# Kernel tuning notes

Measured on AMD Instinct MI355X. Metric: run time of the kernel, lower is better.

Reference implementation:

```python
import jax, jax.numpy as jnp
import numpy as np

B, DIM, HEADS, H, W = 4, 64, 64, 256, 256


def _conv1x1(x, w):
    # x: [b,c,h,w], w: [o,c] -> [b,o,h,w]
    return jnp.einsum('bchw,oc->bohw', x, w)


def _conv3x3_s2_reflect(x, w, groups):
    # reflect pad 1, 3x3 conv, stride 2 (matches padding_mode='reflect', stride=2)
    xp = jnp.pad(x, ((0, 0), (0, 0), (1, 1), (1, 1)), mode='reflect')
    return jax.lax.conv_general_dilated(
        xp, w, window_strides=(2, 2), padding='VALID',
        dimension_numbers=('NCHW', 'OIHW', 'NCHW'), feature_group_count=groups)


def _to_heads(t, heads):
    # safe_rearrange: zero-pad channels to a multiple of heads, then b (head c) h w -> b head c (h w)
    b, c, h, w = t.shape
    if c % heads != 0:
        t = jnp.pad(t, ((0, 0), (0, heads - c % heads), (0, 0), (0, 0)))
        c = t.shape[1]
    return t.reshape(b, heads, c // heads, h * w)


def _l2norm(t, eps=1e-12):
    # F.normalize(dim=-1): x / max(||x||, eps)
    n = jnp.sqrt(jnp.sum(t * t, axis=-1, keepdims=True))
    return t / jnp.maximum(n, eps)


def setup_inputs() -> dict:
    key = jax.random.key(0)
    ks = jax.random.split(key, 13)
    d = DIM
    s = 0.05
    return {
        'x': jax.random.normal(ks[0], (B, d, H, W), jnp.float32),
        'illu_feat': jax.random.uniform(ks[1], (B, d, H, W), jnp.float32),
        'w_q_spec': jax.random.normal(ks[2], (d, d), jnp.float32) * s,
        'w_k_spec': jax.random.normal(ks[3], (d, d), jnp.float32) * s,
        'w_v_spec': jax.random.normal(ks[4], (d, d), jnp.float32) * s,
        'w_q_spat': jax.random.normal(ks[5], (d, 1, 3, 3), jnp.float32) * s,  # depthwise
        'w_k_spat': jax.random.normal(ks[6], (d, d, 3, 3), jnp.float32) * s,
        'w_v_spat': jax.random.normal(ks[7], (d, d), jnp.float32) * s,
        'w_anchor_dw': jax.random.normal(ks[8], (d, 1, 3, 3), jnp.float32) * s,  # depthwise
        'w_anchor_pw': jax.random.normal(ks[9], (d // 2, d), jnp.float32) * s,
        'w_proj': jax.random.normal(ks[10], (d, d), jnp.float32) * s,
        'temp_spec': jnp.ones((HEADS, 1, 1), jnp.float32),
        'temp_spat': jnp.ones((HEADS, 1, 1), jnp.float32),
    }


def reference(x, illu_feat, w_q_spec, w_k_spec, w_v_spec, w_q_spat, w_k_spat,
              w_v_spat, w_anchor_dw, w_anchor_pw, w_proj, temp_spec, temp_spat):
    b, c, h, w = x.shape
    heads = HEADS

    q_spec = _conv1x1(x, w_q_spec)
    k_spec = _conv1x1(x, w_k_spec)                       # computed but unused downstream (as in original)
    v_spec = _conv1x1(x, w_v_spec) * illu_feat
    q_spat = _conv3x3_s2_reflect(x, w_q_spat, groups=c)  # computed but unused downstream (as in original)
    k_spat = _conv3x3_s2_reflect(x, w_k_spat, groups=1)
    v_spat = _conv1x1(x, w_v_spat) * illu_feat
    anchor = _conv1x1(_conv3x3_s2_reflect(x, w_anchor_dw, groups=c), w_anchor_pw)

    q_spec = _l2norm(_to_heads(q_spec, heads))
    k_spec = _l2norm(_to_heads(k_spec, heads))
    v_spec = _to_heads(v_spec, heads)
    q_spat = _l2norm(_to_heads(q_spat, heads))
    k_spat = _to_heads(k_spat, heads)
    v_spat = _to_heads(v_spat, heads)
    anchor = _l2norm(_to_heads(anchor, heads))

    n_q = q_spec.shape[-1]      # h*w
    n_a = anchor.shape[-1]      # (h//2)*(w//2)
    n_v = v_spec.shape[-1]
    n_k = k_spat.shape[-1]

    # spectral branch: q x anchor (truncate to common spatial length)
    m = min(n_q, n_a)
    attn_spec = jnp.einsum('bhcn,bhdn->bhcd', q_spec[..., :m], anchor[..., :m]) * temp_spec
    attn_spec = jax.nn.softmax(attn_spec, axis=-1)

    # v_spec spatial matching via adaptive avg pool (static no-op here since n_v == n_q)
    if n_v != n_q:
        vh = int(n_v ** 0.5)
        qh = int(n_q ** 0.5)
        v4 = v_spec.reshape(b, heads, v_spec.shape[2], vh, vh)
        v4 = jax.image.resize(v4, (b, heads, v_spec.shape[2], qh, qh), method='linear')
        v_spec_matched = v4.reshape(b, heads, v_spec.shape[2], -1)
    else:
        v_spec_matched = v_spec

    # spatial branch: anchor x k_spat (truncate to common spatial length)
    m2 = min(n_a, n_k)
    attn_spat = jnp.einsum('bhcn,bhdn->bhcd', anchor[..., :m2], k_spat[..., :m2]) * temp_spat
    attn_spat = jax.nn.softmax(attn_spat, axis=-1)

    out_spec = jnp.einsum('bhcd,bhdn->bhcn', attn_spec, v_spec_matched)
    out_spat = jnp.einsum('bhcd,bhdn->bhcn', attn_spat, v_spat)

    m3 = min(out_spec.shape[-1], out_spat.shape[-1])
    out = 0.6 * out_spec[..., :m3] + 0.4 * out_spat[..., :m3]

    ah = int(m3 ** 0.5)
    out = out.reshape(b, heads * out.shape[2], ah, ah)
    if ah != h or ah != w:
        # F.interpolate bilinear, align_corners=False == half-pixel linear resize
        out = jax.image.resize(out, (b, out.shape[1], h, w), method='bilinear')
    out = out[:, :DIM]
    return _conv1x1(out, w_proj)
```

## Files before the change

kernel.cpp:

```cpp
#include <hip/hip_runtime.h>


#define HW    65536
#define CHHW  (64 * 65536)
#define PT    128
#define SXT   68
#define SIL   132
#define TPB   4

typedef short s4_t __attribute__((ext_vector_type(4)));
typedef short s8_t __attribute__((ext_vector_type(8)));
typedef float f4_t __attribute__((ext_vector_type(4)));

static __device__ __forceinline__ unsigned short f2bf(float f) {
  unsigned u = __float_as_uint(f);
  return (unsigned short)((u + 0x7fffu + ((u >> 16) & 1u)) >> 16);
}
static __device__ __forceinline__ s8_t ld8(const unsigned short* p) {
  s4_t lo = *(const s4_t*)p;
  s4_t hi = *(const s4_t*)(p + 4);
  s8_t r = {lo[0], lo[1], lo[2], lo[3], hi[0], hi[1], hi[2], hi[3]};
  return r;
}

__global__ __launch_bounds__(256, 2) void fused_hsattn(
    const float* __restrict__ x, const float* __restrict__ illu,
    const float* __restrict__ wvs, const float* __restrict__ wvt,
    const float* __restrict__ wproj, float* __restrict__ out) {
  __shared__ __align__(16) unsigned short WM[64 * SXT];
  __shared__ __align__(16) unsigned short WP[64 * SXT];
  __shared__ __align__(16) unsigned short XT[PT * SXT];
  __shared__ __align__(16) float ILS[64 * SIL];

  const int tid  = threadIdx.x;
  const int lane = tid & 63;
  const int wv   = tid >> 6;
  const int n15  = lane & 15;
  const int q    = lane >> 4;

  const int ch0 = wv * 16 + (lane >> 5);
  const int pxl = (lane & 31) * 4;

  f4_t wa[4], wb[4], wc[4];
#pragma unroll
  for (int it = 0; it < 4; ++it) {
    int j4 = (it * 256 + tid) * 4;
    wa[it] = *(const f4_t*)(wvs + j4);
    wb[it] = *(const f4_t*)(wvt + j4);
    wc[it] = *(const f4_t*)(wproj + j4);
  }

  f4_t xr[8], ir[8];
  {
    const int g    = blockIdx.x * TPB;
    const int base = (g >> 9) * CHHW + ((g & 511) << 7);
#pragma unroll
    for (int it = 0; it < 8; ++it) {
      const int off = base + (ch0 + 2 * it) * HW + pxl;
      xr[it] = *(const f4_t*)(x + off);
      ir[it] = *(const f4_t*)(illu + off);
    }
  }

#pragma unroll
  for (int it = 0; it < 4; ++it) {
    int idx = it * 256 + tid;
    int r = idx >> 4, c4 = (idx & 15) * 4;
    s4_t m, w;
#pragma unroll
    for (int j = 0; j < 4; ++j) {
      m[j] = (short)f2bf(0.6f * wa[it][j] + 0.4f * wb[it][j]);
      w[j] = (short)f2bf(wc[it][j]);
    }
    *(s4_t*)(WM + r * SXT + c4) = m;
    *(s4_t*)(WP + r * SXT + c4) = w;
  }

#pragma unroll
  for (int t = 0; t < TPB; ++t) {
    const int g    = blockIdx.x * TPB + t;
    const int base = (g >> 9) * CHHW + ((g & 511) << 7);

#pragma unroll
    for (int it = 0; it < 8; ++it) {
      const int ch = ch0 + 2 * it;
      f4_t v = xr[it];
#pragma unroll
      for (int j = 0; j < 4; ++j)
        XT[(pxl + j) * SXT + ch] = f2bf(v[j]);
      *(f4_t*)(ILS + ch * SIL + pxl) = ir[it];
    }
    __syncthreads();

    if (t + 1 < TPB) {
      const int g2 = g + 1;
      const int b2 = (g2 >> 9) * CHHW + ((g2 & 511) << 7);
#pragma unroll
      for (int it = 0; it < 8; ++it) {
        const int off = b2 + (ch0 + 2 * it) * HW + pxl;
        xr[it] = *(const f4_t*)(x + off);
        ir[it] = *(const f4_t*)(illu + off);
      }
    }

#pragma unroll
    for (int nt = 0; nt < 2; ++nt) {
      const int pr = wv * 32 + nt * 16;
      unsigned short* xrow = XT + (pr + n15) * SXT;

      f4_t acc[4];
#pragma unroll
      for (int i = 0; i < 4; ++i) acc[i] = (f4_t){0.f, 0.f, 0.f, 0.f};
#pragma unroll
      for (int kc = 0; kc < 2; ++kc) {
        s8_t B = ld8(xrow + kc * 32 + q * 8);
#pragma unroll
        for (int mt = 0; mt < 4; ++mt) {
          s8_t A = ld8(WM + (mt * 16 + n15) * SXT + kc * 32 + q * 8);
          acc[mt] = __builtin_amdgcn_mfma_f32_16x16x32_bf16(A, B, acc[mt], 0, 0, 0);
        }
      }

#pragma unroll
      for (int mt = 0; mt < 4; ++mt) {
        s4_t h;
#pragma unroll
        for (int r = 0; r < 4; ++r) {
          const int c = mt * 16 + q * 4 + r;
          h[r] = (short)f2bf(acc[mt][r] * ILS[c * SIL + pr + n15]);
        }
        *(s4_t*)(xrow + mt * 16 + q * 4) = h;
      }

      f4_t acc2[4];
#pragma unroll
      for (int i = 0; i < 4; ++i) acc2[i] = (f4_t){0.f, 0.f, 0.f, 0.f};
#pragma unroll
      for (int kc = 0; kc < 2; ++kc) {
        s8_t B = ld8(xrow + kc * 32 + q * 8);
#pragma unroll
        for (int mt = 0; mt < 4; ++mt) {
          s8_t A = ld8(WP + (mt * 16 + n15) * SXT + kc * 32 + q * 8);
          acc2[mt] = __builtin_amdgcn_mfma_f32_16x16x32_bf16(A, B, acc2[mt], 0, 0, 0);
        }
      }

#pragma unroll
      for (int mt = 0; mt < 4; ++mt) {
        float* op = out + base + (mt * 16 + q * 4) * HW + pr + n15;
        f4_t a = acc2[mt];
#pragma unroll
        for (int r = 0; r < 4; ++r) op[r * HW] = a[r];
      }
    }
    __syncthreads();
  }
}

extern "C" void kernel_launch(void* const* d_in, const int* in_sizes, int n_in,
                              void* d_out, int out_size, void* d_ws, size_t ws_size,
                              hipStream_t stream) {
  const float* x     = (const float*)d_in[0];
  const float* illu  = (const float*)d_in[1];
  const float* wvs   = (const float*)d_in[4];
  const float* wvt   = (const float*)d_in[7];
  const float* wproj = (const float*)d_in[10];
  float* out = (float*)d_out;

  fused_hsattn<<<(4 * (HW / PT)) / TPB, 256, 0, stream>>>(x, illu, wvs, wvt,
                                                          wproj, out);
}
```

Measured before the change: 203.3 us.

## Load MFMA operands directly from global into registers, dropping shared staging

After: 252.7 us. +24.3%, slower.

```diff
diff --git a/kernel.cpp b/kernel.cpp
--- a/kernel.cpp
+++ b/kernel.cpp
@@ -3,10 +3,10 @@
 
 #define HW    65536
 #define CHHW  (64 * 65536)
-#define PT    128
 #define SXT   68
-#define SIL   132
-#define TPB   4
+#define WPX   32
+#define BPX   128
+#define TPB   2
 
 typedef short s4_t __attribute__((ext_vector_type(4)));
 typedef short s8_t __attribute__((ext_vector_type(8)));
@@ -23,23 +23,20 @@
   return r;
 }
 
-__global__ __launch_bounds__(256, 2) void fused_hsattn(
+__global__ __launch_bounds__(256, 4) void fused_hsattn(
     const float* __restrict__ x, const float* __restrict__ illu,
     const float* __restrict__ wvs, const float* __restrict__ wvt,
     const float* __restrict__ wproj, float* __restrict__ out) {
   __shared__ __align__(16) unsigned short WM[64 * SXT];
   __shared__ __align__(16) unsigned short WP[64 * SXT];
-  __shared__ __align__(16) unsigned short XT[PT * SXT];
-  __shared__ __align__(16) float ILS[64 * SIL];
+  __shared__ __align__(16) unsigned short XH[BPX * SXT];
 
   const int tid  = threadIdx.x;
   const int lane = tid & 63;
   const int wv   = tid >> 6;
   const int n15  = lane & 15;
   const int q    = lane >> 4;
-
-  const int ch0 = wv * 16 + (lane >> 5);
-  const int pxl = (lane & 31) * 4;
+  const int wpx  = wv * WPX;
 
   f4_t wa[4], wb[4], wc[4];
 #pragma unroll
@@ -48,18 +45,6 @@
     wa[it] = *(const f4_t*)(wvs + j4);
     wb[it] = *(const f4_t*)(wvt + j4);
     wc[it] = *(const f4_t*)(wproj + j4);
-  }
-
-  f4_t xr[8], ir[8];
-  {
-    const int g    = blockIdx.x * TPB;
-    const int base = (g >> 9) * CHHW + ((g & 511) << 7);
-#pragma unroll
-    for (int it = 0; it < 8; ++it) {
-      const int off = base + (ch0 + 2 * it) * HW + pxl;
-      xr[it] = *(const f4_t*)(x + off);
-      ir[it] = *(const f4_t*)(illu + off);
-    }
   }
 
 #pragma unroll
@@ -75,85 +60,112 @@
     *(s4_t*)(WM + r * SXT + c4) = m;
     *(s4_t*)(WP + r * SXT + c4) = w;
   }
+  __syncthreads();
+
+  unsigned short* xr0 = XH + (wpx + n15) * SXT;
+  unsigned short* xr1 = XH + (wpx + 16 + n15) * SXT;
 
 #pragma unroll
   for (int t = 0; t < TPB; ++t) {
     const int g    = blockIdx.x * TPB + t;
     const int base = (g >> 9) * CHHW + ((g & 511) << 7);
 
+    const float* xb = x + base + wpx + n15;
+    const float* ib = illu + base + wpx + n15;
+    float xv0[16], xv1[16], iv0[16], iv1[16];
 #pragma unroll
-    for (int it = 0; it < 8; ++it) {
-      const int ch = ch0 + 2 * it;
-      f4_t v = xr[it];
+    for (int kc = 0; kc < 2; ++kc)
 #pragma unroll
-      for (int j = 0; j < 4; ++j)
-        XT[(pxl + j) * SXT + ch] = f2bf(v[j]);
-      *(f4_t*)(ILS + ch * SIL + pxl) = ir[it];
+      for (int j = 0; j < 8; ++j) {
+        xv0[kc * 8 + j] = xb[(kc * 32 + q * 8 + j) * HW];
+        xv1[kc * 8 + j] = xb[(kc * 32 + q * 8 + j) * HW + 16];
+      }
+#pragma unroll
+    for (int mt = 0; mt < 4; ++mt)
+#pragma unroll
+      for (int r = 0; r < 4; ++r) {
+        iv0[mt * 4 + r] = ib[(mt * 16 + q * 4 + r) * HW];
+        iv1[mt * 4 + r] = ib[(mt * 16 + q * 4 + r) * HW + 16];
+      }
+
+    s8_t B00, B01, B10, B11;
+#pragma unroll
+    for (int j = 0; j < 8; ++j) {
+      B00[j] = (short)f2bf(xv0[j]);
+      B01[j] = (short)f2bf(xv0[8 + j]);
+      B10[j] = (short)f2bf(xv1[j]);
+      B11[j] = (short)f2bf(xv1[8 + j]);
     }
-    __syncthreads();
 
-    if (t + 1 < TPB) {
-      const int g2 = g + 1;
-      const int b2 = (g2 >> 9) * CHHW + ((g2 & 511) << 7);
+    {
+      f4_t acc[4];
 #pragma unroll
-      for (int it = 0; it < 8; ++it) {
-        const int off = b2 + (ch0 + 2 * it) * HW + pxl;
-        xr[it] = *(const f4_t*)(x + off);
-        ir[it] = *(const f4_t*)(illu + off);
+      for (int i = 0; i < 4; ++i) acc[i] = (f4_t){0.f, 0.f, 0.f, 0.f};
+#pragma unroll
+      for (int mt = 0; mt < 4; ++mt) {
+        s8_t A0 = ld8(WM + (mt * 16 + n15) * SXT + q * 8);
+        acc[mt] = __builtin_amdgcn_mfma_f32_16x16x32_bf16(A0, B00, acc[mt], 0, 0, 0);
+        s8_t A1 = ld8(WM + (mt * 16 + n15) * SXT + 32 + q * 8);
+        acc[mt] = __builtin_amdgcn_mfma_f32_16x16x32_bf16(A1, B01, acc[mt], 0, 0, 0);
+      }
+#pragma unroll
+      for (int mt = 0; mt < 4; ++mt) {
+        s4_t h;
+#pragma unroll
+        for (int r = 0; r < 4; ++r)
+          h[r] = (short)f2bf(acc[mt][r] * iv0[mt * 4 + r]);
+        *(s4_t*)(xr0 + mt * 16 + q * 4) = h;
+      }
+    }
+
+    {
+      f4_t acc[4];
+#pragma unroll
+      for (int i = 0; i < 4; ++i) acc[i] = (f4_t){0.f, 0.f, 0.f, 0.f};
+#pragma unroll
+      for (int mt = 0; mt < 4; ++mt) {
+        s8_t A0 = ld8(WM + (mt * 16 + n15) * SXT + q * 8);
+        acc[mt] = __builtin_amdgcn_mfma_f32_16x16x32_bf16(A0, B10, acc[mt], 0, 0, 0);
+        s8_t A1 = ld8(WM + (mt * 16 + n15) * SXT + 32 + q * 8);
+        acc[mt] = __builtin_amdgcn_mfma_f32_16x16x32_bf16(A1, B11, acc[mt], 0, 0, 0);
+      }
+#pragma unroll
+      for (int mt = 0; mt < 4; ++mt) {
+        s4_t h;
+#pragma unroll
+        for (int r = 0; r < 4; ++r)
+          h[r] = (short)f2bf(acc[mt][r] * iv1[mt * 4 + r]);
+        *(s4_t*)(xr1 + mt * 16 + q * 4) = h;
+      }
+    }
+
+    f4_t a20[4], a21[4];
+#pragma unroll
+    for (int i = 0; i < 4; ++i) {
+      a20[i] = (f4_t){0.f, 0.f, 0.f, 0.f};
+      a21[i] = (f4_t){0.f, 0.f, 0.f, 0.f};
+    }
+#pragma unroll
+    for (int kc = 0; kc < 2; ++kc) {
+      s8_t Bn0 = ld8(xr0 + kc * 32 + q * 8);
+      s8_t Bn1 = ld8(xr1 + kc * 32 + q * 8);
+#pragma unroll
+      for (int mt = 0; mt < 4; ++mt) {
+        s8_t A = ld8(WP + (mt * 16 + n15) * SXT + kc * 32 + q * 8);
+        a20[mt] = __builtin_amdgcn_mfma_f32_16x16x32_bf16(A, Bn0, a20[mt], 0, 0, 0);
+        a21[mt] = __builtin_amdgcn_mfma_f32_16x16x32_bf16(A, Bn1, a21[mt], 0, 0, 0);
       }
     }
 
 #pragma unroll
-    for (int nt = 0; nt < 2; ++nt) {
-      const int pr = wv * 32 + nt * 16;
-      unsigned short* xrow = XT + (pr + n15) * SXT;
-
-      f4_t acc[4];
+    for (int mt = 0; mt < 4; ++mt) {
+      float* op = out + base + (mt * 16 + q * 4) * HW + wpx + n15;
 #pragma unroll
-      for (int i = 0; i < 4; ++i) acc[i] = (f4_t){0.f, 0.f, 0.f, 0.f};
-#pragma unroll
-      for (int kc = 0; kc < 2; ++kc) {
-        s8_t B = ld8(xrow + kc * 32 + q * 8);
-#pragma unroll
-        for (int mt = 0; mt < 4; ++mt) {
-          s8_t A = ld8(WM + (mt * 16 + n15) * SXT + kc * 32 + q * 8);
-          acc[mt] = __builtin_amdgcn_mfma_f32_16x16x32_bf16(A, B, acc[mt], 0, 0, 0);
-        }
-      }
-
-#pragma unroll
-      for (int mt = 0; mt < 4; ++mt) {
-        s4_t h;
-#pragma unroll
-        for (int r = 0; r < 4; ++r) {
-          const int c = mt * 16 + q * 4 + r;
-          h[r] = (short)f2bf(acc[mt][r] * ILS[c * SIL + pr + n15]);
-        }
-        *(s4_t*)(xrow + mt * 16 + q * 4) = h;
-      }
-
-      f4_t acc2[4];
-#pragma unroll
-      for (int i = 0; i < 4; ++i) acc2[i] = (f4_t){0.f, 0.f, 0.f, 0.f};
-#pragma unroll
-      for (int kc = 0; kc < 2; ++kc) {
-        s8_t B = ld8(xrow + kc * 32 + q * 8);
-#pragma unroll
-        for (int mt = 0; mt < 4; ++mt) {
-          s8_t A = ld8(WP + (mt * 16 + n15) * SXT + kc * 32 + q * 8);
-          acc2[mt] = __builtin_amdgcn_mfma_f32_16x16x32_bf16(A, B, acc2[mt], 0, 0, 0);
-        }
-      }
-
-#pragma unroll
-      for (int mt = 0; mt < 4; ++mt) {
-        float* op = out + base + (mt * 16 + q * 4) * HW + pr + n15;
-        f4_t a = acc2[mt];
-#pragma unroll
-        for (int r = 0; r < 4; ++r) op[r * HW] = a[r];
+      for (int r = 0; r < 4; ++r) {
+        op[r * HW]      = a20[mt][r];
+        op[r * HW + 16] = a21[mt][r];
       }
     }
-    __syncthreads();
   }
 }
 
@@ -167,6 +179,6 @@
   const float* wproj = (const float*)d_in[10];
   float* out = (float*)d_out;
 
-  fused_hsattn<<<(4 * (HW / PT)) / TPB, 256, 0, stream>>>(x, illu, wvs, wvt,
-                                                          wproj, out);
+  fused_hsattn<<<(4 * (HW / BPX)) / TPB, 256, 0, stream>>>(x, illu, wvs, wvt,
+                                                           wproj, out);
 }
```
